# Kernel tuning notes

Hardware: AMD Instinct MI355X
Metric: run time of the kernel (lower is better)

Reference implementation:

```python
import jax, jax.numpy as jnp
import numpy as np

B, S, D, L = 2, 1024, 1024, 8
HQ, HK, DH = 16, 4, 64          # query heads, kv heads, head_dim = D // HQ
FF, V = 2816, 32000             # FFN hidden (2/3*4D rounded to 256), vocab
EPS = 1e-5
THETA = 500000.0


def setup_inputs() -> dict:
    key = jax.random.key(0)
    ks = jax.random.split(key, 12)
    s = 0.02
    n = lambda k, sh: jax.random.normal(k, sh, dtype=jnp.float32) * s
    return {
        "tokens": jax.random.randint(ks[0], (B, S), 0, V),
        "start_pos": 0,
        "tok_emb": n(ks[1], (V, D)),
        "wq": n(ks[2], (L, D, HQ * DH)),
        "wk": n(ks[3], (L, D, HK * DH)),
        "wv": n(ks[4], (L, D, HK * DH)),
        "wo": n(ks[5], (L, HQ * DH, D)),
        "w1": n(ks[6], (L, D, FF)),
        "w2": n(ks[7], (L, FF, D)),
        "w3": n(ks[8], (L, D, FF)),
        "attn_norm_w": jnp.ones((L, D), jnp.float32),
        "ffn_norm_w": jnp.ones((L, D), jnp.float32),
        "final_norm_w": jnp.ones((D,), jnp.float32),
        "out_w": n(ks[9], (D, V)),
    }


def _rope_cos_sin(start, seqlen):
    freqs = 1.0 / (THETA ** (jnp.arange(0, DH, 2, dtype=jnp.float32) / DH))  # [DH/2]
    t = jnp.arange(start, start + seqlen, dtype=jnp.float32)
    ang = jnp.outer(t, freqs)  # [S, DH/2]
    return jnp.cos(ang), jnp.sin(ang)


def _apply_rope(x, cos, sin):
    # x: [B,S,H,DH]; pairs (even, odd) rotated by complex freqs_cis, as in apply_rotary_emb
    xr = x.reshape(x.shape[:-1] + (DH // 2, 2))
    a, b = xr[..., 0], xr[..., 1]
    c = cos[None, :, None, :]
    s = sin[None, :, None, :]
    out = jnp.stack([a * c - b * s, a * s + b * c], axis=-1)
    return out.reshape(x.shape)


def _rmsnorm(x, w):
    return x * jax.lax.rsqrt(jnp.mean(x * x, axis=-1, keepdims=True) + EPS) * w


def reference(tokens, start_pos, tok_emb, wq, wk, wv, wo, w1, w2, w3,
              attn_norm_w, ffn_norm_w, final_norm_w, out_w):
    h = tok_emb[tokens]  # [B,S,D]
    cos, sin = _rope_cos_sin(start_pos, S)
    # strictly-upper-triangular -inf causal mask (seqlen > 1 branch)
    idx = jnp.arange(S)
    mask = jnp.where(idx[None, :] > idx[:, None], -jnp.inf, 0.0).astype(h.dtype)

    def block(h, p):
        wq_, wk_, wv_, wo_, w1_, w2_, w3_, anw, fnw = p
        x = _rmsnorm(h, anw)
        q = (x @ wq_).reshape(B, S, HQ, DH)
        k = (x @ wk_).reshape(B, S, HK, DH)
        v = (x @ wv_).reshape(B, S, HK, DH)
        q = _apply_rope(q, cos, sin)
        k = _apply_rope(k, cos, sin)
        # start_pos=0: cache slice [:, :seqlen] == freshly written k/v; GQA repeat_kv
        k = jnp.repeat(k, HQ // HK, axis=2)  # [B,S,HQ,DH]
        v = jnp.repeat(v, HQ // HK, axis=2)
        scores = jnp.einsum('bqhd,bkhd->bhqk', q, k) / (DH ** 0.5) + mask
        attn = jax.nn.softmax(scores.astype(jnp.float32), axis=-1).astype(q.dtype)
        o = jnp.einsum('bhqk,bkhd->bqhd', attn, v).reshape(B, S, HQ * DH)
        h = h + o @ wo_
        x2 = _rmsnorm(h, fnw)
        ff = (jax.nn.silu(x2 @ w1_) * (x2 @ w3_)) @ w2_
        return h + ff, None

    h, _ = jax.lax.scan(block, h, (wq, wk, wv, wo, w1, w2, w3, attn_norm_w, ffn_norm_w))
    return (_rmsnorm(h, final_norm_w) @ out_w).astype(jnp.float32)
```

## Files before the change

### kernel.cpp

```cpp
#include <hip/hip_runtime.h>
#include <hip/hip_bf16.h>

typedef __bf16 bf16;
typedef __bf16 bf16x8 __attribute__((ext_vector_type(8)));
typedef float f32x4 __attribute__((ext_vector_type(4)));

#define B_ 2
#define S_ 1024
#define D_ 1024
#define L_ 8
#define HQ_ 16
#define HK_ 4
#define DH_ 64
#define FF_ 2816
#define V_ 32000

#define LGKM0 { asm volatile("s_waitcnt lgkmcnt(0)" ::: "memory"); __builtin_amdgcn_sched_barrier(0); }

__global__ __launch_bounds__(256) void embed_k(const int* __restrict__ toks,
                                               const float* __restrict__ emb,
                                               float* __restrict__ h) {
  int row = blockIdx.x;
  int tok = toks[row];
  f32x4 v = *(const f32x4*)&emb[(size_t)tok * D_ + threadIdx.x * 4];
  *(f32x4*)&h[(size_t)row * D_ + threadIdx.x * 4] = v;
}

__global__ __launch_bounds__(256) void ropetab_k(float* __restrict__ tab) {
  int i = blockIdx.x * 256 + threadIdx.x;
  if (i >= S_ * 32) return;
  int d = i & 31, s = i >> 5;
  float f = expf(-(2.0f * d / 64.0f) * logf(500000.0f));
  float ang = (float)s * f;
  tab[i * 2]     = cosf(ang);
  tab[i * 2 + 1] = sinf(ang);
}

__global__ __launch_bounds__(256) void rmsnorm_k(const float* __restrict__ x,
                                                 const float* __restrict__ w,
                                                 bf16* __restrict__ out) {
  int row = blockIdx.x;
  const float* xr = x + (size_t)row * D_;
  int base = threadIdx.x * 4;
  f32x4 v = *(const f32x4*)&xr[base];
  float ss = v[0]*v[0] + v[1]*v[1] + v[2]*v[2] + v[3]*v[3];
  for (int m = 1; m < 64; m <<= 1) ss += __shfl_xor(ss, m, 64);
  __shared__ float partial[4];
  if ((threadIdx.x & 63) == 0) partial[threadIdx.x >> 6] = ss;
  __syncthreads();
  float tot = partial[0] + partial[1] + partial[2] + partial[3];
  float rr = rsqrtf(tot * (1.0f / D_) + 1e-5f);
  f32x4 wv = *(const f32x4*)&w[base];
  bf16* o = out + (size_t)row * D_ + base;
  o[0] = (bf16)(v[0] * rr * wv[0]);
  o[1] = (bf16)(v[1] * rr * wv[1]);
  o[2] = (bf16)(v[2] * rr * wv[2]);
  o[3] = (bf16)(v[3] * rr * wv[3]);
}

__global__ __launch_bounds__(256) void transpose_cvt(const float* __restrict__ src,
                                                     bf16* __restrict__ dst,
                                                     int K, int N,
                                                     long long srcStride, long long dstStride,
                                                     int rowMul, int rowAdd) {
  __shared__ float tile[32][33];
  int bx = blockIdx.x, by = blockIdx.y, z = blockIdx.z;
  src += (size_t)z * srcStride;
  dst += (size_t)z * dstStride;
  int tx = threadIdx.x & 31, ty = threadIdx.x >> 5;
#pragma unroll
  for (int i = 0; i < 4; ++i) {
    int r = ty + i * 8;
    tile[r][tx] = src[(size_t)(by * 32 + r) * N + bx * 32 + tx];
  }
  __syncthreads();
#pragma unroll
  for (int i = 0; i < 4; ++i) {
    int r = ty + i * 8;
    dst[(size_t)((bx * 32 + r) * rowMul + rowAdd) * K + by * 32 + tx] = (bf16)tile[tx][r];
  }
}

template <int EPI, int BM>
__global__ __launch_bounds__(256) void gemm_bt(const bf16* __restrict__ A,
                                               const bf16* __restrict__ BT,
                                               void* __restrict__ Cout,
                                               const float* __restrict__ R,
                                               int M, int N, int K,
                                               int lda, int ldb,
                                               int zKoff, long long partStride) {
  constexpr int MR = BM / 32;
  __shared__ bf16 As[BM * 64];
  __shared__ bf16 Bs[128 * 64];
  const int t = threadIdx.x;
  const int w = t >> 6, l = t & 63;
  const int l15 = l & 15, l4 = l >> 4;
  const int bm = blockIdx.x * BM, bn = blockIdx.y * 128;
  const int wr = w >> 1, wc = w & 1;
  const int z = blockIdx.z;

  const bf16* Az = A + (size_t)z * zKoff;
  const bf16* Bz = BT + (size_t)z * zKoff;
  float* Cz = (float*)Cout + (size_t)z * partStride;

  const int srow = t >> 3, scol = (t & 7) * 8;
  const bf16* ag = &Az[(size_t)(bm + srow) * lda + scol];
  const bf16* bg = &Bz[(size_t)(bn + srow) * ldb + scol];
  const int ldsbase = (t & 192) * 8;

  f32x4 acc[MR][4] = {};

  for (int k0 = 0; k0 < K; k0 += 64) {
#pragma unroll
    for (int i = 0; i < BM / 32; ++i)
      __builtin_amdgcn_global_load_lds(
          (const __attribute__((address_space(1))) void*)(ag + (size_t)(i * 32) * lda + k0),
          (__attribute__((address_space(3))) void*)&As[i * 2048 + ldsbase], 16, 0, 0);
#pragma unroll
    for (int i = 0; i < 4; ++i)
      __builtin_amdgcn_global_load_lds(
          (const __attribute__((address_space(1))) void*)(bg + (size_t)(i * 32) * ldb + k0),
          (__attribute__((address_space(3))) void*)&Bs[i * 2048 + ldsbase], 16, 0, 0);
    __syncthreads();
#pragma unroll
    for (int kc = 0; kc < 2; ++kc) {
      bf16x8 af[MR], bfr[4];
#pragma unroll
      for (int m = 0; m < MR; ++m)
        af[m] = *(const bf16x8*)&As[(wr * (BM / 2) + m * 16 + l15) * 64 + kc * 32 + l4 * 8];
#pragma unroll
      for (int n = 0; n < 4; ++n)
        bfr[n] = *(const bf16x8*)&Bs[(wc * 64 + n * 16 + l15) * 64 + kc * 32 + l4 * 8];
#pragma unroll
      for (int m = 0; m < MR; ++m)
#pragma unroll
        for (int n = 0; n < 4; ++n)
          acc[m][n] = __builtin_amdgcn_mfma_f32_16x16x32_bf16(af[m], bfr[n], acc[m][n], 0, 0, 0);
    }
    __syncthreads();
  }

#pragma unroll
  for (int m = 0; m < MR; ++m)
#pragma unroll
    for (int n = 0; n < 4; ++n)
#pragma unroll
      for (int r = 0; r < 4; ++r) {
        int row = bm + wr * (BM / 2) + m * 16 + l4 * 4 + r;
        int col = bn + wc * 64 + n * 16 + l15;
        size_t ix = (size_t)row * N + col;
        float v = acc[m][n][r];
        if (EPI == 0)      Cz[ix] = v;
        else               Cz[ix] = v + R[ix];
      }
}

__global__ __launch_bounds__(256) void reduce2_k(const float* __restrict__ p,
                                                 float* __restrict__ h) {
  size_t i = ((size_t)blockIdx.x * 256 + threadIdx.x) * 4;
  f32x4 a = *(const f32x4*)&p[i];
  f32x4 b = *(const f32x4*)&p[i + 2097152];
  f32x4 r = *(const f32x4*)&h[i];
  r += a + b;
  *(f32x4*)&h[i] = r;
}

template <int EPI>
__global__ __launch_bounds__(512, 2) void gemm256_bt(const bf16* __restrict__ A,
                                                     const bf16* __restrict__ BT,
                                                     void* __restrict__ Cout,
                                                     const float* __restrict__ R,
                                                     int N, int K) {
  extern __shared__ char smem[];
  const int t = threadIdx.x;
  const int wid = t >> 6, l = t & 63;
  const int l15 = l & 15, l4 = l >> 4;
  const int wr = wid >> 2, wc = wid & 3;
  const int rsw = (l4 ^ ((l15 >> 1) & 3)) * 16;
  const int csw = ((t & 3) ^ ((t >> 3) & 3)) * 8;

  int nwg = gridDim.x;
  int q = nwg >> 3, r = nwg & 7;
  int xcd = blockIdx.x & 7, jj = blockIdx.x >> 3;
  int L = (xcd < r ? xcd * (q + 1) : r * (q + 1) + (xcd - r) * q) + jj;
  const int bm = (L & 7) * 256, bn = (L >> 3) * 256;

  const int NT = K >> 6;

  auto stage = [&](const bf16* __restrict__ G, int rowbase, int cbase, int buf, int kc, int kt) {
#pragma unroll
    for (int i = 0; i < 2; ++i) {
      int j = i * 512 + t;
      const bf16* src = G + (size_t)(rowbase + (j >> 2)) * K + kt * 64 + kc * 32 + csw;
      __builtin_amdgcn_global_load_lds(
          (const __attribute__((address_space(1))) void*)src,
          (__attribute__((address_space(3))) void*)(smem + cbase + buf * 32768 + kc * 16384 +
                                                    i * 8192 + wid * 1024),
          16, 0, 0);
    }
  };
  auto ldA = [&](int buf, int kc, int m) -> bf16x8 {
    return *(const bf16x8*)(smem + buf * 32768 + kc * 16384 +
                            (wr * 128 + m * 16 + l15) * 64 + rsw);
  };
  auto ldB = [&](int buf, int kc, int n) -> bf16x8 {
    return *(const bf16x8*)(smem + 65536 + buf * 32768 + kc * 16384 +
                            (wc * 64 + n * 16 + l15) * 64 + rsw);
  };

  f32x4 acc[8][4] = {};
  bf16x8 af[4], bq[4];

  auto rd03 = [&](int buf, int kc) {
#pragma unroll
    for (int m = 0; m < 4; ++m) af[m] = ldA(buf, kc, m);
#pragma unroll
    for (int n = 0; n < 4; ++n) bq[n] = ldB(buf, kc, n);
  };
  auto rd47 = [&](int buf, int kc) {
#pragma unroll
    for (int m = 0; m < 4; ++m) af[m] = ldA(buf, kc, 4 + m);
  };
  auto mf_lo = [&]() {
    __builtin_amdgcn_s_setprio(1);
#pragma unroll
    for (int m = 0; m < 4; ++m)
#pragma unroll
      for (int n = 0; n < 4; ++n)
        acc[m][n] = __builtin_amdgcn_mfma_f32_16x16x32_bf16(af[m], bq[n], acc[m][n], 0, 0, 0);
    __builtin_amdgcn_s_setprio(0);
    __builtin_amdgcn_sched_barrier(0);
  };
  auto mf_hi = [&]() {
    __builtin_amdgcn_s_setprio(1);
#pragma unroll
    for (int m = 0; m < 4; ++m)
#pragma unroll
      for (int n = 0; n < 4; ++n)
        acc[4 + m][n] = __builtin_amdgcn_mfma_f32_16x16x32_bf16(af[m], bq[n], acc[4 + m][n], 0, 0, 0);
    __builtin_amdgcn_s_setprio(0);
    __builtin_amdgcn_sched_barrier(0);
  };
#define GBAR { __builtin_amdgcn_sched_barrier(0); __builtin_amdgcn_s_barrier(); }
#define VMW(n) { asm volatile("s_waitcnt vmcnt(" #n ")" ::: "memory"); __builtin_amdgcn_sched_barrier(0); }

  stage(A, bm, 0, 0, 0, 0);  stage(BT, bn, 65536, 0, 0, 0);
  stage(A, bm, 0, 0, 1, 0);  stage(BT, bn, 65536, 0, 1, 0);
  stage(A, bm, 0, 1, 0, 1);  stage(BT, bn, 65536, 1, 0, 1);
  VMW(8);
  __builtin_amdgcn_s_barrier();

  for (int kt = 0; kt < NT - 2; ++kt) {
    const int buf = kt & 1, nbuf = buf ^ 1;
    rd03(buf, 0);
    stage(A, bm, 0, nbuf, 1, kt + 1);
    GBAR; mf_lo(); GBAR;
    rd47(buf, 0);
    stage(BT, bn, 65536, nbuf, 1, kt + 1);
    GBAR; mf_hi(); VMW(8); __builtin_amdgcn_s_barrier();
    rd03(buf, 1);
    stage(A, bm, 0, buf, 0, kt + 2);
    stage(BT, bn, 65536, buf, 0, kt + 2);
    GBAR; mf_lo(); GBAR;
    rd47(buf, 1);
    GBAR; mf_hi(); VMW(8); __builtin_amdgcn_s_barrier();
  }
  {
    const int kt = NT - 2;
    const int buf = kt & 1, nbuf = buf ^ 1;
    rd03(buf, 0);
    stage(A, bm, 0, nbuf, 1, kt + 1);
    GBAR; mf_lo(); GBAR;
    rd47(buf, 0);
    stage(BT, bn, 65536, nbuf, 1, kt + 1);
    GBAR; mf_hi(); VMW(8); __builtin_amdgcn_s_barrier();
    rd03(buf, 1);
    GBAR; mf_lo(); GBAR;
    rd47(buf, 1);
    GBAR; mf_hi(); VMW(4); __builtin_amdgcn_s_barrier();
  }
  {
    const int buf = (NT - 1) & 1;
    rd03(buf, 0);
    GBAR; mf_lo(); GBAR;
    rd47(buf, 0);
    GBAR; mf_hi(); VMW(0); __builtin_amdgcn_s_barrier();
    rd03(buf, 1);
    GBAR; mf_lo(); GBAR;
    rd47(buf, 1);
    GBAR; mf_hi(); __builtin_amdgcn_s_barrier();
  }
#undef GBAR
#undef VMW

#pragma unroll
  for (int m = 0; m < 8; ++m)
#pragma unroll
    for (int n = 0; n < 4; ++n)
#pragma unroll
      for (int rr = 0; rr < 4; ++rr) {
        int row = bm + wr * 128 + m * 16 + l4 * 4 + rr;
        int col = bn + wc * 64 + n * 16 + l15;
        size_t ix = (size_t)row * N + col;
        float v = acc[m][n][rr];
        if (EPI == 0)      ((float*)Cout)[ix] = v;
        else if (EPI == 1) ((float*)Cout)[ix] = v + R[ix];
        else               ((bf16*)Cout)[ix] = (bf16)v;
      }
}

template <int EPI>
__global__ __launch_bounds__(512, 4) void gemm8_bt(const bf16* __restrict__ A,
                                                   const bf16* __restrict__ BT,
                                                   void* __restrict__ Cout,
                                                   const float* __restrict__ R,
                                                   int N, int K) {
  extern __shared__ char smem[];
  const int t = threadIdx.x;
  const int wid = t >> 6, l = t & 63;
  const int l15 = l & 15, l4 = l >> 4;
  const int wr = wid >> 1, wc = wid & 1;
  const int rsw = (l4 ^ ((l15 >> 1) & 3)) * 16;
  const int csw = ((t & 3) ^ ((t >> 3) & 3)) * 8;

  int nwg = gridDim.x;
  int q = nwg >> 3;
  int xcd = blockIdx.x & 7, jj = blockIdx.x >> 3;
  int L = xcd * q + jj;
  const int bm = (L & 15) * 128, bn = (L >> 4) * 128;

  const int NT = K >> 6;

  auto stage = [&](const bf16* __restrict__ G, int rowbase, int obase, int buf, int kc, int kt) {
    const bf16* src = G + (size_t)(rowbase + (t >> 2)) * K + kt * 64 + kc * 32 + csw;
    __builtin_amdgcn_global_load_lds(
        (const __attribute__((address_space(1))) void*)src,
        (__attribute__((address_space(3))) void*)(smem + obase + buf * 16384 + kc * 8192 +
                                                  wid * 1024),
        16, 0, 0);
  };
  auto ldA = [&](int buf, int kc, int m) -> bf16x8 {
    return *(const bf16x8*)(smem + buf * 16384 + kc * 8192 +
                            (wr * 32 + m * 16 + l15) * 64 + rsw);
  };
  auto ldB = [&](int buf, int kc, int n) -> bf16x8 {
    return *(const bf16x8*)(smem + 32768 + buf * 16384 + kc * 8192 +
                            (wc * 64 + n * 16 + l15) * 64 + rsw);
  };

  f32x4 acc[2][4] = {};
  bf16x8 af[2], bq[4];

  auto rdph = [&](int buf, int kc) {
#pragma unroll
    for (int m = 0; m < 2; ++m) af[m] = ldA(buf, kc, m);
#pragma unroll
    for (int n = 0; n < 4; ++n) bq[n] = ldB(buf, kc, n);
  };
  auto mf = [&]() {
    __builtin_amdgcn_s_setprio(1);
#pragma unroll
    for (int m = 0; m < 2; ++m)
#pragma unroll
      for (int n = 0; n < 4; ++n)
        acc[m][n] = __builtin_amdgcn_mfma_f32_16x16x32_bf16(af[m], bq[n], acc[m][n], 0, 0, 0);
    __builtin_amdgcn_s_setprio(0);
    __builtin_amdgcn_sched_barrier(0);
  };
#define SCB __builtin_amdgcn_sched_barrier(0)
#define VMW4 { asm volatile("s_waitcnt vmcnt(4)" ::: "memory"); SCB; }
#define VMW2 { asm volatile("s_waitcnt vmcnt(2)" ::: "memory"); SCB; }
#define VMW0 { asm volatile("s_waitcnt vmcnt(0)" ::: "memory"); SCB; }
#define SBAR { __builtin_amdgcn_s_barrier(); SCB; }

  stage(A, bm, 0, 0, 0, 0);  stage(BT, bn, 32768, 0, 0, 0);
  stage(A, bm, 0, 0, 1, 0);  stage(BT, bn, 32768, 0, 1, 0);
  stage(A, bm, 0, 1, 0, 1);  stage(BT, bn, 32768, 1, 0, 1);
  VMW4; __builtin_amdgcn_s_barrier();

  for (int kt = 0; kt < NT - 2; ++kt) {
    const int buf = kt & 1, nbuf = buf ^ 1;
    rdph(buf, 0);
    stage(A, bm, 0, nbuf, 1, kt + 1);
    stage(BT, bn, 32768, nbuf, 1, kt + 1);
    SCB; mf(); VMW4; SBAR;
    rdph(buf, 1);
    stage(A, bm, 0, buf, 0, kt + 2);
    stage(BT, bn, 32768, buf, 0, kt + 2);
    SCB; mf(); VMW4; SBAR;
  }
  {
    const int buf = (NT - 2) & 1, nbuf = buf ^ 1;
    rdph(buf, 0);
    stage(A, bm, 0, nbuf, 1, NT - 1);
    stage(BT, bn, 32768, nbuf, 1, NT - 1);
    SCB; mf(); VMW4; SBAR;
    rdph(buf, 1);
    SCB; mf(); VMW2; SBAR;
  }
  {
    const int buf = (NT - 1) & 1;
    rdph(buf, 0);
    SCB; mf(); VMW0; SBAR;
    rdph(buf, 1);
    SCB; mf();
  }
#undef SCB
#undef VMW4
#undef VMW2
#undef VMW0
#undef SBAR

  if (EPI == 3) {
    bf16* G = (bf16*)Cout;
    const int Nc = N >> 1;
#pragma unroll
    for (int m = 0; m < 2; ++m)
#pragma unroll
      for (int n = 0; n < 4; ++n)
#pragma unroll
        for (int rr = 0; rr < 4; ++rr) {
          float v = acc[m][n][rr];
          float part = __shfl_xor(v, 1, 64);
          if (!(l15 & 1)) {
            float a = v, c = part;
            float s = a / (1.0f + __expf(-a));
            int row = bm + wr * 32 + m * 16 + l4 * 4 + rr;
            int col = (bn >> 1) + wc * 32 + n * 8 + (l15 >> 1);
            G[(size_t)row * Nc + col] = (bf16)(s * c);
          }
        }
  } else {
#pragma unroll
    for (int m = 0; m < 2; ++m)
#pragma unroll
      for (int n = 0; n < 4; ++n)
#pragma unroll
        for (int rr = 0; rr < 4; ++rr) {
          int row = bm + wr * 32 + m * 16 + l4 * 4 + rr;
          int col = bn + wc * 64 + n * 16 + l15;
          size_t ix = (size_t)row * N + col;
          float v = acc[m][n][rr];
          if (EPI == 0)      ((float*)Cout)[ix] = v;
          else               ((bf16*)Cout)[ix] = (bf16)v;
        }
  }
}

__global__ __launch_bounds__(256) void qkvpost_k(const bf16* __restrict__ qkv,
                                                 const float* __restrict__ tab,
                                                 bf16* __restrict__ q_r,
                                                 bf16* __restrict__ k_r,
                                                 bf16* __restrict__ vT) {
  int bid = blockIdx.x, t = threadIdx.x;
  if (bid < 1024) {
    int i = bid * 256 + t;
    int g = i & 7, hh = (i >> 3) & 15, s = (i >> 7) & 1023, b = i >> 17;
    bf16x8 v = *(const bf16x8*)&qkv[(size_t)(b * S_ + s) * 1536 + hh * 64 + g * 8];
    f32x4 tc0 = *(const f32x4*)&tab[(s * 32 + g * 4) * 2];
    f32x4 tc1 = *(const f32x4*)&tab[(s * 32 + g * 4) * 2 + 4];
    bf16x8 o;
#pragma unroll
    for (int j = 0; j < 4; ++j) {
      float a = (float)v[2 * j], bb = (float)v[2 * j + 1];
      float c  = (j < 2 ? tc0 : tc1)[(j & 1) * 2];
      float sn = (j < 2 ? tc0 : tc1)[(j & 1) * 2 + 1];
      o[2 * j]     = (bf16)((a * c - bb * sn) * 0.125f);
      o[2 * j + 1] = (bf16)((a * sn + bb * c) * 0.125f);
    }
    *(bf16x8*)&q_r[((size_t)((b * HQ_ + hh) * S_ + s)) * 64 + g * 8] = o;
  } else if (bid < 1280) {
    int i = (bid - 1024) * 256 + t;
    int g = i & 7, hh = (i >> 3) & 3, s = (i >> 5) & 1023, b = i >> 15;
    bf16x8 v = *(const bf16x8*)&qkv[(size_t)(b * S_ + s) * 1536 + 1024 + hh * 64 + g * 8];
    f32x4 tc0 = *(const f32x4*)&tab[(s * 32 + g * 4) * 2];
    f32x4 tc1 = *(const f32x4*)&tab[(s * 32 + g * 4) * 2 + 4];
    bf16x8 o;
#pragma unroll
    for (int j = 0; j < 4; ++j) {
      float a = (float)v[2 * j], bb = (float)v[2 * j + 1];
      float c  = (j < 2 ? tc0 : tc1)[(j & 1) * 2];
      float sn = (j < 2 ? tc0 : tc1)[(j & 1) * 2 + 1];
      o[2 * j]     = (bf16)(a * c - bb * sn);
      o[2 * j + 1] = (bf16)(a * sn + bb * c);
    }
    *(bf16x8*)&k_r[((size_t)((b * HK_ + hh) * S_ + s)) * 64 + g * 8] = o;
  } else {
    __shared__ bf16 vt[64][66];
    int vb = bid - 1280;
    int b = vb >> 6, hh = (vb >> 4) & 3, s0 = (vb & 15) * 64;
#pragma unroll
    for (int it = 0; it < 2; ++it) {
      int idx = it * 256 + t;
      int s = idx >> 3, g = idx & 7;
      bf16x8 v = *(const bf16x8*)&qkv[(size_t)(b * S_ + s0 + s) * 1536 + 1280 + hh * 64 + g * 8];
      *(bf16x8*)&vt[s][g * 8] = v;
    }
    __syncthreads();
#pragma unroll
    for (int it = 0; it < 2; ++it) {
      int idx = it * 256 + t;
      int dh = idx >> 3, sg = idx & 7;
      bf16x8 o;
#pragma unroll
      for (int j = 0; j < 8; ++j) o[j] = vt[sg * 8 + j][dh];
      *(bf16x8*)&vT[((size_t)((b * HK_ + hh) * 64 + dh)) * S_ + s0 + sg * 8] = o;
    }
  }
}

__global__ __launch_bounds__(256) void attn_k(const bf16* __restrict__ q_r,
                                              const bf16* __restrict__ k_r,
                                              const bf16* __restrict__ vT,
                                              bf16* __restrict__ o) {
  __shared__ bf16 k_lds[64 * 64];
  __shared__ bf16 v_lds[64 * 64];
  __shared__ bf16 p_lds[4][16 * 72];
  int t = threadIdx.x, w = t >> 6, l = t & 63, l15 = l & 15, l4 = l >> 4;
  int bx = blockIdx.x;
  int qt = bx & 15;
  if (bx >= 256) qt = 15 - qt;
  int head = (bx >> 4) & 15, b = bx >> 8;
  int kvh = head >> 2;
  const bf16* qh = q_r + ((size_t)(b * HQ_ + head)) * S_ * 64;
  const bf16* kh = k_r + ((size_t)(b * HK_ + kvh)) * S_ * 64;
  const bf16* vh = vT + ((size_t)(b * HK_ + kvh)) * 64 * S_;
  int q0 = qt * 64 + w * 16;

  bf16x8 aq[2];
  aq[0] = *(const bf16x8*)&qh[(size_t)(q0 + l15) * 64 + l4 * 8];
  aq[1] = *(const bf16x8*)&qh[(size_t)(q0 + l15) * 64 + 32 + l4 * 8];

  f32x4 acc_o[4] = {};
  float m_run[4], l_run[4];
#pragma unroll
  for (int r = 0; r < 4; ++r) { m_run[r] = -1e30f; l_run[r] = 0.f; }

  bf16x8 gk[2], gv[2];
#pragma unroll
  for (int i = 0; i < 2; ++i) {
    int c = i * 256 + t;
    gk[i] = *(const bf16x8*)&kh[c * 8];
    gv[i] = *(const bf16x8*)&vh[(size_t)(c >> 3) * S_ + (c & 7) * 8];
  }

  const int swz = l15 & 7;

  for (int kt = 0; kt <= qt; ++kt) {
#pragma unroll
    for (int i = 0; i < 2; ++i) {
      int c = i * 256 + t;
      int row = c >> 3, ch = (c & 7) ^ (row & 7);
      *(bf16x8*)&k_lds[row * 64 + ch * 8] = gk[i];
      *(bf16x8*)&v_lds[row * 64 + ch * 8] = gv[i];
    }
    __syncthreads();

    bf16x8 gkn[2], gvn[2];
    if (kt < qt) {
      const bf16* srck = kh + (kt + 1) * 4096;
#pragma unroll
      for (int i = 0; i < 2; ++i) {
        int c = i * 256 + t;
        gkn[i] = *(const bf16x8*)&srck[c * 8];
        gvn[i] = *(const bf16x8*)&vh[(size_t)(c >> 3) * S_ + (kt + 1) * 64 + (c & 7) * 8];
      }
    }

    f32x4 sc[4];
#pragma unroll
    for (int nt = 0; nt < 4; ++nt) {
      f32x4 a = {};
#pragma unroll
      for (int kc = 0; kc < 2; ++kc) {
        bf16x8 bk = *(const bf16x8*)&k_lds[(nt * 16 + l15) * 64 + (((kc * 4 + l4) ^ swz) * 8)];
        a = __builtin_amdgcn_mfma_f32_16x16x32_bf16(aq[kc], bk, a, 0, 0, 0);
      }
      sc[nt] = a;
    }

    bool diag = (kt == qt);
#pragma unroll
    for (int r = 0; r < 4; ++r) {
      float pmax = -1e30f;
#pragma unroll
      for (int nt = 0; nt < 4; ++nt) {
        float s = sc[nt][r];
        if (diag) {
          int kj = nt * 16 + l15;
          int qi = w * 16 + l4 * 4 + r;
          if (kj > qi) s = -1e30f;
        }
        sc[nt][r] = s;
        pmax = fmaxf(pmax, s);
      }
      if (!__all(pmax <= m_run[r] + 8.0f)) {
        float mx = pmax;
        mx = fmaxf(mx, __shfl_xor(mx, 1, 64));
        mx = fmaxf(mx, __shfl_xor(mx, 2, 64));
        mx = fmaxf(mx, __shfl_xor(mx, 4, 64));
        mx = fmaxf(mx, __shfl_xor(mx, 8, 64));
        float mn = fmaxf(m_run[r], mx);
        float scale = __expf(m_run[r] - mn);
        m_run[r] = mn;
        l_run[r] *= scale;
#pragma unroll
        for (int nt = 0; nt < 4; ++nt) acc_o[nt][r] *= scale;
      }
      float rs = 0.f;
#pragma unroll
      for (int nt = 0; nt < 4; ++nt) {
        float p = __expf(sc[nt][r] - m_run[r]);
        sc[nt][r] = p;
        rs += p;
      }
      rs += __shfl_xor(rs, 1, 64);
      rs += __shfl_xor(rs, 2, 64);
      rs += __shfl_xor(rs, 4, 64);
      rs += __shfl_xor(rs, 8, 64);
      l_run[r] += rs;
    }

#pragma unroll
    for (int nt = 0; nt < 4; ++nt)
#pragma unroll
      for (int r = 0; r < 4; ++r)
        p_lds[w][(l4 * 4 + r) * 72 + nt * 16 + l15] = (bf16)sc[nt][r];
    LGKM0;

#pragma unroll
    for (int kc = 0; kc < 2; ++kc) {
      bf16x8 pf = *(const bf16x8*)&p_lds[w][l15 * 72 + kc * 32 + l4 * 8];
#pragma unroll
      for (int nt = 0; nt < 4; ++nt) {
        bf16x8 vf = *(const bf16x8*)&v_lds[(nt * 16 + l15) * 64 + (((kc * 4 + l4) ^ swz) * 8)];
        acc_o[nt] = __builtin_amdgcn_mfma_f32_16x16x32_bf16(pf, vf, acc_o[nt], 0, 0, 0);
      }
    }
    __syncthreads();

#pragma unroll
    for (int i = 0; i < 2; ++i) { gk[i] = gkn[i]; gv[i] = gvn[i]; }
  }

#pragma unroll
  for (int nt = 0; nt < 4; ++nt)
#pragma unroll
    for (int r = 0; r < 4; ++r) {
      float ov = acc_o[nt][r] / l_run[r];
      int s = qt * 64 + w * 16 + l4 * 4 + r;
      o[((size_t)(b * S_ + s)) * D_ + head * 64 + nt * 16 + l15] = (bf16)ov;
    }
}

extern "C" void kernel_launch(void* const* d_in, const int* in_sizes, int n_in,
                              void* d_out, int out_size, void* d_ws, size_t ws_size,
                              hipStream_t stream) {
  const int* tokens  = (const int*)d_in[0];
  const float* tok_emb = (const float*)d_in[2];
  const float* wq = (const float*)d_in[3];
  const float* wk = (const float*)d_in[4];
  const float* wv = (const float*)d_in[5];
  const float* wo = (const float*)d_in[6];
  const float* w1 = (const float*)d_in[7];
  const float* w2 = (const float*)d_in[8];
  const float* w3 = (const float*)d_in[9];
  const float* anw = (const float*)d_in[10];
  const float* fnw = (const float*)d_in[11];
  const float* finw = (const float*)d_in[12];
  const float* outw = (const float*)d_in[13];

  (void)hipFuncSetAttribute((const void*)gemm256_bt<0>,
                            hipFuncAttributeMaxDynamicSharedMemorySize, 131072);
  (void)hipFuncSetAttribute((const void*)gemm8_bt<2>,
                            hipFuncAttributeMaxDynamicSharedMemorySize, 65536);
  (void)hipFuncSetAttribute((const void*)gemm8_bt<3>,
                            hipFuncAttributeMaxDynamicSharedMemorySize, 65536);

  auto al = [](size_t x) { return (x + 255) & ~(size_t)255; };
  const size_t WTB   = 11272192ull * 2;
  const size_t OUTWTB = (size_t)V_ * D_ * 2;
  const size_t HB   = (size_t)B_ * S_ * D_ * 4;
  const size_t XBB  = (size_t)B_ * S_ * D_ * 2;
  const size_t QKVB = (size_t)B_ * S_ * 1536 * 2;
  const size_t QRB  = (size_t)B_ * HQ_ * S_ * 64 * 2;
  const size_t KRB  = (size_t)B_ * HK_ * S_ * 64 * 2;
  const size_t OB   = (size_t)B_ * S_ * D_ * 2;
  const size_t GATEB = (size_t)B_ * S_ * 2816 * 2;
  const size_t TABB = (size_t)S_ * 32 * 2 * 4;
  const size_t PARTB = (size_t)B_ * S_ * D_ * 4 * 2;

  size_t fixed = al(OUTWTB) + al(HB) + al(XBB) + al(QKVB) + al(QRB) + al(KRB) + al(KRB) +
                 al(OB) + al(GATEB) + al(TABB) + al(PARTB);
  bool allup = ws_size >= fixed + 8 * al(WTB) + 4096;
  int nslots = allup ? 8 : 1;

  char* p = (char*)d_ws;
  bf16* wT    = (bf16*)p; p += (size_t)nslots * al(WTB);
  bf16* outwT = (bf16*)p; p += al(OUTWTB);
  float* h    = (float*)p; p += al(HB);
  bf16* xb    = (bf16*)p; p += al(XBB);
  bf16* qkv   = (bf16*)p; p += al(QKVB);
  bf16* q_r   = (bf16*)p; p += al(QRB);
  bf16* k_r   = (bf16*)p; p += al(KRB);
  bf16* vTb   = (bf16*)p; p += al(KRB);
  bf16* ob    = (bf16*)p; p += al(OB);
  bf16* gate  = (bf16*)p; p += al(GATEB);
  float* tab  = (float*)p; p += al(TABB);
  float* part = (float*)p; p += al(PARTB);

  const size_t WTS = al(WTB) / 2;
  const size_t OFF_QKV = 0;
  const size_t OFF_WK  = 1024ull * 1024;
  const size_t OFF_WV  = 1280ull * 1024;
  const size_t OFF_WO  = 1572864ull;
  const size_t OFF_W13 = 2621440ull;
  const size_t OFF_W2  = 8388608ull;

  auto tr = [&](const float* src, size_t srcStride, bf16* dst, size_t dstStride,
                int Kd, int Nd, int layers, int rowMul, int rowAdd) {
    transpose_cvt<<<dim3(Nd / 32, Kd / 32, layers), 256, 0, stream>>>(
        src, dst, Kd, Nd, (long long)srcStride, (long long)dstStride, rowMul, rowAdd);
  };

  ropetab_k<<<128, 256, 0, stream>>>(tab);
  embed_k<<<B_ * S_, 256, 0, stream>>>(tokens, tok_emb, h);
  tr(outw, 0, outwT, 0, 1024, 32000, 1, 1, 0);

  if (allup) {
    tr(wq, 1024 * 1024, wT + OFF_QKV, WTS, 1024, 1024, 8, 1, 0);
    tr(wk, 1024 * 256,  wT + OFF_WK,  WTS, 1024, 256, 8, 1, 0);
    tr(wv, 1024 * 256,  wT + OFF_WV,  WTS, 1024, 256, 8, 1, 0);
    tr(wo, 1024 * 1024, wT + OFF_WO,  WTS, 1024, 1024, 8, 1, 0);
    tr(w1, 1024 * 2816, wT + OFF_W13, WTS, 1024, 2816, 8, 2, 0);
    tr(w3, 1024 * 2816, wT + OFF_W13, WTS, 1024, 2816, 8, 2, 1);
    tr(w2, 2816 * 1024, wT + OFF_W2,  WTS, 2816, 1024, 8, 1, 0);
  }

  for (int l = 0; l < L_; ++l) {
    bf16* wtl = wT + (allup ? (size_t)l * WTS : 0);
    if (!allup) {
      tr(wq + (size_t)l * 1024 * 1024, 0, wtl + OFF_QKV, 0, 1024, 1024, 1, 1, 0);
      tr(wk + (size_t)l * 1024 * 256,  0, wtl + OFF_WK,  0, 1024, 256, 1, 1, 0);
      tr(wv + (size_t)l * 1024 * 256,  0, wtl + OFF_WV,  0, 1024, 256, 1, 1, 0);
      tr(wo + (size_t)l * 1024 * 1024, 0, wtl + OFF_WO,  0, 1024, 1024, 1, 1, 0);
      tr(w1 + (size_t)l * 1024 * 2816, 0, wtl + OFF_W13, 0, 1024, 2816, 1, 2, 0);
      tr(w3 + (size_t)l * 1024 * 2816, 0, wtl + OFF_W13, 0, 1024, 2816, 1, 2, 1);
      tr(w2 + (size_t)l * 2816 * 1024, 0, wtl + OFF_W2,  0, 2816, 1024, 1, 1, 0);
    }

    rmsnorm_k<<<B_ * S_, 256, 0, stream>>>(h, anw + l * D_, xb);
    gemm8_bt<2><<<192, 512, 65536, stream>>>(xb, wtl + OFF_QKV, qkv, nullptr, 1536, 1024);
    qkvpost_k<<<1408, 256, 0, stream>>>(qkv, tab, q_r, k_r, vTb);
    attn_k<<<B_ * HQ_ * (S_ / 64), 256, 0, stream>>>(q_r, k_r, vTb, ob);
    gemm_bt<1, 64><<<dim3(32, 8, 1), 256, 0, stream>>>(ob, wtl + OFF_WO, h, h,
                                                       2048, 1024, 1024, 1024, 1024, 0, 0);
    rmsnorm_k<<<B_ * S_, 256, 0, stream>>>(h, fnw + l * D_, xb);
    gemm8_bt<3><<<704, 512, 65536, stream>>>(xb, wtl + OFF_W13, gate, nullptr, 5632, 1024);
    gemm_bt<0, 64><<<dim3(32, 8, 2), 256, 0, stream>>>(gate, wtl + OFF_W2, part, nullptr,
                                                       2048, 1024, 1408, 2816, 2816,
                                                       1408, 2097152ll);
    reduce2_k<<<2048, 256, 0, stream>>>(part, h);
  }

  rmsnorm_k<<<B_ * S_, 256, 0, stream>>>(h, finw, xb);
  gemm256_bt<0><<<1000, 512, 131072, stream>>>(xb, outwT, d_out, nullptr, 32000, 1024);
}
```

Measured before the change: 1.537 ms.

## Fuse split-K reduce with next RMSNorm, widen attention KV tiles to 128

Replaces the split-K reduction kernel and the following RMSNorm with one kernel that adds the partial sums into the residual and directly produces the next layer's (or the final) normalized bf16 input. Attention now processes 128 keys per iteration instead of 64, halving loop trips and barriers at the cost of more LDS and registers and some wasted masked work on the diagonal tile. The output-projection GEMM switches to a smaller tile with twice as many blocks to improve occupancy.

```diff
diff --git a/kernel.cpp b/kernel.cpp
--- a/kernel.cpp
+++ b/kernel.cpp
@@ -58,6 +58,33 @@
   o[3] = (bf16)(v[3] * rr * wv[3]);
 }
 
+__global__ __launch_bounds__(256) void redrms_k(const float* __restrict__ p,
+                                                float* __restrict__ h,
+                                                const float* __restrict__ w,
+                                                bf16* __restrict__ out) {
+  int row = blockIdx.x;
+  int base = threadIdx.x * 4;
+  size_t ix = (size_t)row * D_ + base;
+  f32x4 a = *(const f32x4*)&p[ix];
+  f32x4 bb = *(const f32x4*)&p[ix + 2097152];
+  f32x4 v = *(const f32x4*)&h[ix];
+  v += a + bb;
+  *(f32x4*)&h[ix] = v;
+  float ss = v[0]*v[0] + v[1]*v[1] + v[2]*v[2] + v[3]*v[3];
+  for (int m = 1; m < 64; m <<= 1) ss += __shfl_xor(ss, m, 64);
+  __shared__ float partial[4];
+  if ((threadIdx.x & 63) == 0) partial[threadIdx.x >> 6] = ss;
+  __syncthreads();
+  float tot = partial[0] + partial[1] + partial[2] + partial[3];
+  float rr = rsqrtf(tot * (1.0f / D_) + 1e-5f);
+  f32x4 wv = *(const f32x4*)&w[base];
+  bf16* o = out + (size_t)row * D_ + base;
+  o[0] = (bf16)(v[0] * rr * wv[0]);
+  o[1] = (bf16)(v[1] * rr * wv[1]);
+  o[2] = (bf16)(v[2] * rr * wv[2]);
+  o[3] = (bf16)(v[3] * rr * wv[3]);
+}
+
 __global__ __launch_bounds__(256) void transpose_cvt(const float* __restrict__ src,
                                                      bf16* __restrict__ dst,
                                                      int K, int N,
@@ -155,16 +182,6 @@
       }
 }
 
-__global__ __launch_bounds__(256) void reduce2_k(const float* __restrict__ p,
-                                                 float* __restrict__ h) {
-  size_t i = ((size_t)blockIdx.x * 256 + threadIdx.x) * 4;
-  f32x4 a = *(const f32x4*)&p[i];
-  f32x4 b = *(const f32x4*)&p[i + 2097152];
-  f32x4 r = *(const f32x4*)&h[i];
-  r += a + b;
-  *(f32x4*)&h[i] = r;
-}
-
 template <int EPI>
 __global__ __launch_bounds__(512, 2) void gemm256_bt(const bf16* __restrict__ A,
                                                      const bf16* __restrict__ BT,
@@ -513,9 +530,9 @@
                                               const bf16* __restrict__ k_r,
                                               const bf16* __restrict__ vT,
                                               bf16* __restrict__ o) {
-  __shared__ bf16 k_lds[64 * 64];
-  __shared__ bf16 v_lds[64 * 64];
-  __shared__ bf16 p_lds[4][16 * 72];
+  __shared__ bf16 k_lds[128 * 64];
+  __shared__ bf16 v_lds[64 * 128];
+  __shared__ bf16 p_lds[4][16 * 136];
   int t = threadIdx.x, w = t >> 6, l = t & 63, l15 = l & 15, l4 = l >> 4;
   int bx = blockIdx.x;
   int qt = bx & 15;
@@ -526,6 +543,7 @@
   const bf16* kh = k_r + ((size_t)(b * HK_ + kvh)) * S_ * 64;
   const bf16* vh = vT + ((size_t)(b * HK_ + kvh)) * 64 * S_;
   int q0 = qt * 64 + w * 16;
+  const int ntile = (qt + 2) >> 1;
 
   bf16x8 aq[2];
   aq[0] = *(const bf16x8*)&qh[(size_t)(q0 + l15) * 64 + l4 * 8];
@@ -536,59 +554,58 @@
 #pragma unroll
   for (int r = 0; r < 4; ++r) { m_run[r] = -1e30f; l_run[r] = 0.f; }
 
-  bf16x8 gk[2], gv[2];
-#pragma unroll
-  for (int i = 0; i < 2; ++i) {
+  bf16x8 gk[4], gv[4];
+#pragma unroll
+  for (int i = 0; i < 4; ++i) {
     int c = i * 256 + t;
-    gk[i] = *(const bf16x8*)&kh[c * 8];
-    gv[i] = *(const bf16x8*)&vh[(size_t)(c >> 3) * S_ + (c & 7) * 8];
-  }
-
-  const int swz = l15 & 7;
-
-  for (int kt = 0; kt <= qt; ++kt) {
-#pragma unroll
-    for (int i = 0; i < 2; ++i) {
+    gk[i] = *(const bf16x8*)&kh[(size_t)(c >> 3) * 64 + (c & 7) * 8];
+    gv[i] = *(const bf16x8*)&vh[(size_t)(c >> 4) * S_ + (c & 15) * 8];
+  }
+
+  for (int j = 0; j < ntile; ++j) {
+#pragma unroll
+    for (int i = 0; i < 4; ++i) {
       int c = i * 256 + t;
-      int row = c >> 3, ch = (c & 7) ^ (row & 7);
-      *(bf16x8*)&k_lds[row * 64 + ch * 8] = gk[i];
-      *(bf16x8*)&v_lds[row * 64 + ch * 8] = gv[i];
+      int krow = c >> 3, kch = (c & 7) ^ (krow & 7);
+      *(bf16x8*)&k_lds[krow * 64 + kch * 8] = gk[i];
+      int vrow = c >> 4, vch = (c & 15) ^ (vrow & 15);
+      *(bf16x8*)&v_lds[vrow * 128 + vch * 8] = gv[i];
     }
     __syncthreads();
 
-    bf16x8 gkn[2], gvn[2];
-    if (kt < qt) {
-      const bf16* srck = kh + (kt + 1) * 4096;
-#pragma unroll
-      for (int i = 0; i < 2; ++i) {
+    bf16x8 gkn[4], gvn[4];
+    if (j + 1 < ntile) {
+#pragma unroll
+      for (int i = 0; i < 4; ++i) {
         int c = i * 256 + t;
-        gkn[i] = *(const bf16x8*)&srck[c * 8];
-        gvn[i] = *(const bf16x8*)&vh[(size_t)(c >> 3) * S_ + (kt + 1) * 64 + (c & 7) * 8];
+        gkn[i] = *(const bf16x8*)&kh[(size_t)((j + 1) * 128 + (c >> 3)) * 64 + (c & 7) * 8];
+        gvn[i] = *(const bf16x8*)&vh[(size_t)(c >> 4) * S_ + (j + 1) * 128 + (c & 15) * 8];
       }
     }
 
-    f32x4 sc[4];
-#pragma unroll
-    for (int nt = 0; nt < 4; ++nt) {
+    f32x4 sc[8];
+#pragma unroll
+    for (int nt = 0; nt < 8; ++nt) {
       f32x4 a = {};
 #pragma unroll
       for (int kc = 0; kc < 2; ++kc) {
-        bf16x8 bk = *(const bf16x8*)&k_lds[(nt * 16 + l15) * 64 + (((kc * 4 + l4) ^ swz) * 8)];
+        bf16x8 bk = *(const bf16x8*)&k_lds[(nt * 16 + l15) * 64 +
+                                           (((kc * 4 + l4) ^ (l15 & 7)) * 8)];
         a = __builtin_amdgcn_mfma_f32_16x16x32_bf16(aq[kc], bk, a, 0, 0, 0);
       }
       sc[nt] = a;
     }
 
-    bool diag = (kt == qt);
+    bool lastt = (j == ntile - 1);
 #pragma unroll
     for (int r = 0; r < 4; ++r) {
       float pmax = -1e30f;
 #pragma unroll
-      for (int nt = 0; nt < 4; ++nt) {
+      for (int nt = 0; nt < 8; ++nt) {
         float s = sc[nt][r];
-        if (diag) {
-          int kj = nt * 16 + l15;
-          int qi = w * 16 + l4 * 4 + r;
+        if (lastt) {
+          int kj = j * 128 + nt * 16 + l15;
+          int qi = q0 + l4 * 4 + r;
           if (kj > qi) s = -1e30f;
         }
         sc[nt][r] = s;
@@ -609,7 +626,7 @@
       }
       float rs = 0.f;
 #pragma unroll
-      for (int nt = 0; nt < 4; ++nt) {
+      for (int nt = 0; nt < 8; ++nt) {
         float p = __expf(sc[nt][r] - m_run[r]);
         sc[nt][r] = p;
         rs += p;
@@ -622,25 +639,26 @@
     }
 
 #pragma unroll
-    for (int nt = 0; nt < 4; ++nt)
+    for (int nt = 0; nt < 8; ++nt)
 #pragma unroll
       for (int r = 0; r < 4; ++r)
-        p_lds[w][(l4 * 4 + r) * 72 + nt * 16 + l15] = (bf16)sc[nt][r];
+        p_lds[w][(l4 * 4 + r) * 136 + nt * 16 + l15] = (bf16)sc[nt][r];
     LGKM0;
 
 #pragma unroll
-    for (int kc = 0; kc < 2; ++kc) {
-      bf16x8 pf = *(const bf16x8*)&p_lds[w][l15 * 72 + kc * 32 + l4 * 8];
+    for (int kc = 0; kc < 4; ++kc) {
+      bf16x8 pf = *(const bf16x8*)&p_lds[w][l15 * 136 + kc * 32 + l4 * 8];
 #pragma unroll
       for (int nt = 0; nt < 4; ++nt) {
-        bf16x8 vf = *(const bf16x8*)&v_lds[(nt * 16 + l15) * 64 + (((kc * 4 + l4) ^ swz) * 8)];
+        bf16x8 vf = *(const bf16x8*)&v_lds[(nt * 16 + l15) * 128 +
+                                           (((kc * 4 + l4) ^ l15) * 8)];
         acc_o[nt] = __builtin_amdgcn_mfma_f32_16x16x32_bf16(pf, vf, acc_o[nt], 0, 0, 0);
       }
     }
     __syncthreads();
 
 #pragma unroll
-    for (int i = 0; i < 2; ++i) { gk[i] = gkn[i]; gv[i] = gvn[i]; }
+    for (int i = 0; i < 4; ++i) { gk[i] = gkn[i]; gv[i] = gvn[i]; }
   }
 
 #pragma unroll
@@ -737,6 +755,8 @@
     tr(w2, 2816 * 1024, wT + OFF_W2,  WTS, 2816, 1024, 8, 1, 0);
   }
 
+  rmsnorm_k<<<B_ * S_, 256, 0, stream>>>(h, anw, xb);
+
   for (int l = 0; l < L_; ++l) {
     bf16* wtl = wT + (allup ? (size_t)l * WTS : 0);
     if (!allup) {
@@ -749,20 +769,19 @@
       tr(w2 + (size_t)l * 2816 * 1024, 0, wtl + OFF_W2,  0, 2816, 1024, 1, 1, 0);
     }
 
-    rmsnorm_k<<<B_ * S_, 256, 0, stream>>>(h, anw + l * D_, xb);
     gemm8_bt<2><<<192, 512, 65536, stream>>>(xb, wtl + OFF_QKV, qkv, nullptr, 1536, 1024);
     qkvpost_k<<<1408, 256, 0, stream>>>(qkv, tab, q_r, k_r, vTb);
     attn_k<<<B_ * HQ_ * (S_ / 64), 256, 0, stream>>>(q_r, k_r, vTb, ob);
-    gemm_bt<1, 64><<<dim3(32, 8, 1), 256, 0, stream>>>(ob, wtl + OFF_WO, h, h,
+    gemm_bt<1, 32><<<dim3(64, 8, 1), 256, 0, stream>>>(ob, wtl + OFF_WO, h, h,
                                                        2048, 1024, 1024, 1024, 1024, 0, 0);
     rmsnorm_k<<<B_ * S_, 256, 0, stream>>>(h, fnw + l * D_, xb);
     gemm8_bt<3><<<704, 512, 65536, stream>>>(xb, wtl + OFF_W13, gate, nullptr, 5632, 1024);
     gemm_bt<0, 64><<<dim3(32, 8, 2), 256, 0, stream>>>(gate, wtl + OFF_W2, part, nullptr,
                                                        2048, 1024, 1408, 2816, 2816,
                                                        1408, 2097152ll);
-    reduce2_k<<<2048, 256, 0, stream>>>(part, h);
-  }
-
-  rmsnorm_k<<<B_ * S_, 256, 0, stream>>>(h, finw, xb);
+    redrms_k<<<B_ * S_, 256, 0, stream>>>(part, h,
+                                          (l < L_ - 1) ? (anw + (l + 1) * D_) : finw, xb);
+  }
+
   gemm256_bt<0><<<1000, 512, 131072, stream>>>(xb, outwT, d_out, nullptr, 32000, 1024);
 }
```

Result: faster. 1.477 ms (-3.9%).
